# Performance work log

Hardware: AMD Instinct MI355X
Metric: run time of the kernel (lower is better)

## Reference

```python
import jax, jax.numpy as jnp
import numpy as np

B, T, J, V, D, H = 32, 400, 30, 50000, 150, 150
L = 2  # answer_token_len (boundary model: start, end)


def _gru_step(h, x, Wih, Whh, bih, bhh):
    # torch GRUCell semantics
    gi = x @ Wih.T + bih
    gh = h @ Whh.T + bhh
    ir, iz, inn = jnp.split(gi, 3, axis=-1)
    hr, hz, hn = jnp.split(gh, 3, axis=-1)
    r = jax.nn.sigmoid(ir + hr)
    z = jax.nn.sigmoid(iz + hz)
    n = jnp.tanh(inn + r * hn)
    return (1.0 - z) * n + z * h


def _gru_seq(x, Wih, Whh, bih, bhh):
    # x: [B, S, din] -> hidden sequence [B, S, h]
    h0 = jnp.zeros((x.shape[0], Whh.shape[1]), x.dtype)
    def step(h, xt):
        h = _gru_step(h, xt, Wih, Whh, bih, bhh)
        return h, h
    _, hs = jax.lax.scan(step, h0, jnp.swapaxes(x, 0, 1))
    return jnp.swapaxes(hs, 0, 1)


def _forward(context, query,
             E,
             ctx_Wih, ctx_Whh, ctx_bih, ctx_bhh,
             q_Wih, q_Whh, q_bih, q_bhh,
             Wq, Wp, Wr, w, gate_bias, attn_bias,
             m_Wih, m_Whh, m_bih, m_bhh,
             mr_Wih, mr_Whh, mr_bih, mr_bhh,
             ptr_W1, ptr_W2, ptr_v,
             d_Wih, d_Whh, d_bih, d_bhh):
    # encode context and query with GRUs
    Hp = _gru_seq(E[context], ctx_Wih, ctx_Whh, ctx_bih, ctx_bhh)  # [B,T,H]
    Hq = _gru_seq(E[query], q_Wih, q_Whh, q_bih, q_bhh)            # [B,J,H]

    whq = jnp.einsum('bjh,hk->bjk', Hq, Wq)  # precomputed query projection [B,J,H]

    def match_scan(xs, cWih, cWhh, cbih, cbhh):
        # xs: [B,T,H] context encodings (possibly time-reversed)
        def step(h, xt):
            # G_i = tanh(Wq Hq + (Wp p_i + Wr h_{i-1}) + bias)  -> [B,J,H]
            g = jnp.tanh(whq + (xt @ Wp + h @ Wr + gate_bias)[:, None, :])
            a = jax.nn.softmax(g @ w + attn_bias, axis=-1)       # [B,J]
            q = jnp.einsum('bj,bjh->bh', a, Hq)                  # attended query
            z = jnp.concatenate([xt, q], axis=-1)                # [B,2H]
            h = _gru_step(h, z, cWih, cWhh, cbih, cbhh)
            return h, h
        h0 = jnp.zeros((xs.shape[0], xs.shape[2]), xs.dtype)
        _, hs = jax.lax.scan(step, h0, jnp.swapaxes(xs, 0, 1))
        return jnp.swapaxes(hs, 0, 1)  # [B,T,H]

    Hf = match_scan(Hp, m_Wih, m_Whh, m_bih, m_bhh)              # forward direction
    Hb = match_scan(Hp[:, ::-1], mr_Wih, mr_Whh, mr_bih, mr_bhh) # reverse direction (scan order, as original)
    Hr = jnp.concatenate([Hf, Hb], axis=-1)                      # [B,T,2H]
    zero0 = jnp.zeros((Hr.shape[0], 1, Hr.shape[2]), Hr.dtype)   # initial zero state prepended
    Hr = jnp.concatenate([zero0, Hr], axis=1)                    # [B,T+1,2H]

    # boundary pointer network: L attention steps over H_r
    enc = Hr @ ptr_W1
    def ptr_step(h, _):
        s = jnp.tanh(enc + (h @ ptr_W2)[:, None, :]) @ ptr_v     # [B,T+1]
        a = jax.nn.softmax(s, axis=-1)
        c = jnp.einsum('bt,bth->bh', a, Hr)
        h = _gru_step(h, c, d_Wih, d_Whh, d_bih, d_bhh)
        return h, a
    h0 = jnp.zeros((Hr.shape[0], Hr.shape[2]), Hr.dtype)
    _, probs = jax.lax.scan(ptr_step, h0, None, length=L)
    return jnp.swapaxes(probs, 0, 1)  # [B, L, T+1]


def setup_inputs() -> dict:
    key = jax.random.key(0)
    keys = iter(jax.random.split(key, 40))
    p = lambda *s: jax.random.normal(next(keys), s, jnp.float32) * 0.05
    inp = {
        'context': jax.random.randint(next(keys), (B, T), 0, V, dtype=jnp.int32),
        'query': jax.random.randint(next(keys), (B, J), 0, V, dtype=jnp.int32),
        'E': p(V, D),
        'ctx_Wih': p(3 * H, D), 'ctx_Whh': p(3 * H, H), 'ctx_bih': p(3 * H), 'ctx_bhh': p(3 * H),
        'q_Wih': p(3 * H, D), 'q_Whh': p(3 * H, H), 'q_bih': p(3 * H), 'q_bhh': p(3 * H),
        'Wq': p(H, H), 'Wp': p(H, H), 'Wr': p(H, H), 'w': p(H),
        'gate_bias': p(H), 'attn_bias': p(),
        'm_Wih': p(3 * H, 2 * H), 'm_Whh': p(3 * H, H), 'm_bih': p(3 * H), 'm_bhh': p(3 * H),
        'mr_Wih': p(3 * H, 2 * H), 'mr_Whh': p(3 * H, H), 'mr_bih': p(3 * H), 'mr_bhh': p(3 * H),
        'ptr_W1': p(2 * H, 2 * H), 'ptr_W2': p(2 * H, 2 * H), 'ptr_v': p(2 * H),
        'd_Wih': p(6 * H, 2 * H), 'd_Whh': p(6 * H, 2 * H), 'd_bih': p(6 * H), 'd_bhh': p(6 * H),
    }
    return inp


def reference(context, query, E,
              ctx_Wih, ctx_Whh, ctx_bih, ctx_bhh,
              q_Wih, q_Whh, q_bih, q_bhh,
              Wq, Wp, Wr, w, gate_bias, attn_bias,
              m_Wih, m_Whh, m_bih, m_bhh,
              mr_Wih, mr_Whh, mr_bih, mr_bhh,
              ptr_W1, ptr_W2, ptr_v,
              d_Wih, d_Whh, d_bih, d_bhh):
    return _forward(context, query, E,
                    ctx_Wih, ctx_Whh, ctx_bih, ctx_bhh,
                    q_Wih, q_Whh, q_bih, q_bhh,
                    Wq, Wp, Wr, w, gate_bias, attn_bias,
                    m_Wih, m_Whh, m_bih, m_bhh,
                    mr_Wih, mr_Whh, mr_bih, mr_bhh,
                    ptr_W1, ptr_W2, ptr_v,
                    d_Wih, d_Whh, d_bih, d_bhh)
```

## Files before the change

### kernel.cpp

```cpp
#include <hip/hip_runtime.h>
#include <hip/hip_bf16.h>


namespace {

constexpr int NBATCH = 32;
constexpr int TLEN   = 400;
constexpr int JQ     = 30;
constexpr int T1     = 401;

__device__ __forceinline__ float sigm(float x){ return 1.f/(1.f+__expf(-x)); }
__device__ __forceinline__ float tanh_f(float x){
  float e = __expf(-2.f*fabsf(x));
  float t = (1.f-e)/(1.f+e);
  return x < 0.f ? -t : t;
}
__device__ __forceinline__ float bf2f(unsigned short u){
  union { unsigned int i; float f; } c; c.i = ((unsigned int)u)<<16; return c.f;
}

__device__ __forceinline__ void bar_lds(){
  asm volatile("s_waitcnt lgkmcnt(0)" ::: "memory");
  __builtin_amdgcn_s_barrier();
}

#define NW 29
struct WDesc { const void* src[NW]; int off[NW+1]; };

__global__ void sniff_kernel(const unsigned int* __restrict__ bits, int* __restrict__ flag){
  __shared__ int cnt;
  if (threadIdx.x==0) cnt = 0;
  __syncthreads();
  int hit = 0;
  #pragma unroll
  for (int i=0;i<4;i++){
    unsigned int w = bits[threadIdx.x*4+i];
    unsigned int b = (w>>8)&0x7Fu;
    if (b==0u || (b>=0x38u && b<=0x3Fu)) hit++;
  }
  atomicAdd(&cnt, hit);
  __syncthreads();
  if (threadIdx.x==0) *flag = (cnt > 768) ? 1 : 0;
}

__global__ void convert_weights_kernel(WDesc d, float* __restrict__ out, const int* __restrict__ flag){
  const int isbf = *flag;
  const int total = d.off[NW];
  for (int e = blockIdx.x*blockDim.x+threadIdx.x; e < total; e += gridDim.x*blockDim.x){
    int j = 0;
    while (e >= d.off[j+1]) j++;
    int i = e - d.off[j];
    out[e] = isbf ? bf2f(((const unsigned short*)d.src[j])[i])
                  : ((const float*)d.src[j])[i];
  }
}

__global__ void padrows_kernel(const float* __restrict__ src, float* __restrict__ dst,
                               int rows, int cols, int ldd){
  int i = blockIdx.x*blockDim.x+threadIdx.x;
  if (i >= rows*ldd) return;
  int r = i/ldd, c = i-r*ldd;
  dst[i] = (c<cols) ? src[(size_t)r*cols+c] : 0.f;
}

__global__ void transpose_kernel(const float* __restrict__ src, float* __restrict__ dst,
                                 int R, int C, int lds_, int offs){
  int idx = blockIdx.x*blockDim.x+threadIdx.x;
  if (idx >= R*C) return;
  int i = idx / R, k = idx - i*R;
  dst[(size_t)i*R + k] = src[(size_t)k*lds_ + offs + i];
}

__global__ void build_wcat_kernel(const float* __restrict__ Whh, const float* __restrict__ Wr,
                                  float* __restrict__ Wcat){
  int i = blockIdx.x*blockDim.x+threadIdx.x;
  if (i >= 600*152) return;
  int r = i/152, c = i-r*152;
  float v = 0.f;
  if (c < 150){
    if (r < 450) v = Whh[(size_t)r*150+c];
    else         v = Wr[(size_t)c*150 + (r-450)];
  }
  Wcat[i] = v;
}

__global__ void build_msplit_kernel(const float* __restrict__ Wcat,
                                    float* __restrict__ s2q, float* __restrict__ ext){
  int i = blockIdx.x*blockDim.x+threadIdx.x;
  if (i < 24576){
    int q = i/2048, rem = i-q*2048, r = rem/4, p = rem-r*4;
    s2q[i] = Wcat[(size_t)r*152 + 104 + 4*q + p];
  } else if (i < 24576+13376){
    int k = i-24576;
    int q = k/352, rem = k-q*352, ii = rem/4, p = rem-ii*4;
    ext[k] = Wcat[(size_t)(512+ii)*152 + 4*q + p];
  }
}

__global__ void build_gsplit_kernel(const float* __restrict__ Wpad, float* __restrict__ s2q){
  int i = blockIdx.x*blockDim.x+threadIdx.x;
  if (i >= 12*452*4) return;
  int q = i/1808, rem = i-q*1808, r = rem/4, p = rem-r*4;
  s2q[i] = (r<450) ? Wpad[(size_t)r*152 + 104 + 4*q + p] : 0.f;
}

__global__ __launch_bounds__(512) void rowproj16_kernel(
    const float* __restrict__ Xrows,
    const int* __restrict__ gather, const void* __restrict__ Etab, const int* __restrict__ bfflag,
    const float* __restrict__ W, const float* __restrict__ bias,
    float* __restrict__ out, int rows, int K, int inner, int ldw, int ldo)
{
  __shared__ __align__(16) float xs[16][304];
  const int r0 = blockIdx.x*16;
  int nr = rows - r0; if (nr > 16) nr = 16;
  if (nr <= 0) return;
  const int isbf = gather ? *bfflag : 0;
  for (int e = threadIdx.x; e < nr*inner; e += 512){
    int r = e/inner, i = e - r*inner;
    float v;
    if (gather){
      size_t base = (size_t)gather[r0+r]*inner + i;
      v = isbf ? bf2f(((const unsigned short*)Etab)[base]) : ((const float*)Etab)[base];
    } else {
      v = Xrows[(size_t)(r0+r)*inner + i];
    }
    xs[r][i] = v;
  }
  __syncthreads();
  for (int k = threadIdx.x; k < K; k += 512){
    float b0 = bias ? bias[k] : 0.f;
    float acc[16];
    #pragma unroll
    for (int r=0;r<16;r++) acc[r] = b0;
    int i = 0;
    for (; i+4 <= inner; i += 4){
      float w0 = W[(size_t)i*ldw + k];
      float w1 = W[(size_t)(i+1)*ldw + k];
      float w2 = W[(size_t)(i+2)*ldw + k];
      float w3 = W[(size_t)(i+3)*ldw + k];
      #pragma unroll
      for (int r=0;r<16;r++){
        float4 xv = *(const float4*)&xs[r][i];
        acc[r] = fmaf(xv.x, w0, acc[r]);
        acc[r] = fmaf(xv.y, w1, acc[r]);
        acc[r] = fmaf(xv.z, w2, acc[r]);
        acc[r] = fmaf(xv.w, w3, acc[r]);
      }
    }
    for (; i < inner; i++){
      float wv = W[(size_t)i*ldw + k];
      #pragma unroll
      for (int r=0;r<16;r++) acc[r] = fmaf(xs[r][i], wv, acc[r]);
    }
    for (int r=0;r<nr;r++) out[(size_t)(r0+r)*ldo + k] = acc[r];
  }
  for (int k = K + threadIdx.x; k < ldo; k += 512)
    for (int r=0;r<nr;r++) out[(size_t)(r0+r)*ldo + k] = 0.f;
}

#define R26(M) M(0) M(1) M(2) M(3) M(4) M(5) M(6) M(7) M(8) M(9) M(10) M(11) \
               M(12) M(13) M(14) M(15) M(16) M(17) M(18) M(19) M(20) M(21) \
               M(22) M(23) M(24) M(25)
#define R12(M) M(26) M(27) M(28) M(29) M(30) M(31) M(32) M(33) M(34) M(35) \
               M(36) M(37)
#define DECW(i) float4 w##i;
#define LDW(i)  w##i = wrow4[i];
#define LDW2(i) w##i = s2q4[(i-26)*s2stride + s2r];
#define FMAW(i) { float4 hq = h4[i]; \
  acc0 = fmaf(hq.x, w##i.x, acc0); acc1 = fmaf(hq.y, w##i.y, acc1); \
  acc2 = fmaf(hq.z, w##i.z, acc2); acc3 = fmaf(hq.w, w##i.w, acc3); }

__global__ __launch_bounds__(512, 2) void gru_scan_kernel(
    const float* __restrict__ gi0, const float* __restrict__ Wp0,
    const float* __restrict__ s2q0, const float* __restrict__ bh0,
    float* __restrict__ H0, int S0,
    const float* __restrict__ gi1, const float* __restrict__ Wp1,
    const float* __restrict__ s2q1, const float* __restrict__ bh1,
    float* __restrict__ H1, int S1)
{
  const int blk = blockIdx.x;
  const float* gi; const float* Wpad; const float* s2qG; const float* bh; float* Hs; int S;
  if (blk < 32){ gi = gi0 + (size_t)blk*S0*450;  Wpad = Wp0; s2qG = s2q0; bh = bh0;
                 Hs = H0 + (size_t)blk*S0*150;   S = S0; }
  else         { int bb = blk-32;
                 gi = gi1 + (size_t)bb*S1*450;   Wpad = Wp1; s2qG = s2q1; bh = bh1;
                 Hs = H1 + (size_t)bb*S1*150;    S = S1; }
  __shared__ __align__(16) float h[152];
  __shared__ float gh[452];
  const int tid = threadIdx.x;

  R26(DECW) R12(DECW)
  float br = 0.f;
  {
    const float4* wrow4 = (const float4*)(Wpad + (size_t)((tid<450)?tid:0)*152);
    R26(LDW)
    const float4* s2q4 = (const float4*)s2qG;
    const int s2stride = 452; const int s2r = (tid<452) ? tid : 0;
    R12(LDW2)
    if (tid<450) br = bh[tid];
  }
  if (tid < 152) h[tid] = 0.f;
  __syncthreads();
  const float4* h4 = (const float4*)h;

  for (int t=0;t<S;t++){
    float g0=0.f,g1=0.f,g2=0.f;
    if (tid < 150){
      const float* gg = gi + (size_t)t*450;
      g0 = gg[tid]; g1 = gg[150+tid]; g2 = gg[300+tid];
    }
    if (tid < 450){
      float acc0=br, acc1=0.f, acc2=0.f, acc3=0.f;
      R26(FMAW) R12(FMAW)
      gh[tid] = (acc0+acc2)+(acc1+acc3);
    }
    bar_lds();
    if (tid < 150){
      float r = sigm(g0 + gh[tid]);
      float z = sigm(g1 + gh[150+tid]);
      float n = tanh_f(g2 + r*gh[300+tid]);
      float hn = (1.f-z)*n + z*h[tid];
      h[tid] = hn;
      Hs[(size_t)t*150 + tid] = hn;
    }
    bar_lds();
  }
}

__global__ void zero_hr0_kernel(float* __restrict__ Hr){
  int idx = blockIdx.x*blockDim.x + threadIdx.x;
  if (idx < NBATCH*300){
    int b = idx/300, k = idx - 300*b;
    Hr[(size_t)b*T1*300 + k] = 0.f;
  }
}

__global__ __launch_bounds__(512, 2) void match_scan_kernel(
    const float* __restrict__ pWp,
    const float* __restrict__ whq,
    const float* __restrict__ giXf,
    const float* __restrict__ giXr,
    const float* __restrict__ Pf,
    const float* __restrict__ Pr,
    const float* __restrict__ WcatF, const float* __restrict__ WcatR,
    const float* __restrict__ s2qF,  const float* __restrict__ s2qR,
    const float* __restrict__ extF,  const float* __restrict__ extR,
    const float* __restrict__ m_bhh, const float* __restrict__ mr_bhh,
    const float* __restrict__ wvec,
    float* __restrict__ Hr)
{
  const int b   = blockIdx.x;
  const int dir = blockIdx.y;
  const float* giX  = dir ? giXr : giXf;
  const float* P    = dir ? Pr   : Pf;
  const float* Wcat = dir ? WcatR : WcatF;
  const float* s2qG = dir ? s2qR  : s2qF;
  const float* extG = dir ? extR  : extF;
  const float* bhh  = dir ? mr_bhh : m_bhh;

  __shared__ float4 extW[3344];
  __shared__ __align__(16) float Ps[JQ*452];
  __shared__ __align__(16) float whqS[JQ*152];
  __shared__ __align__(16) float wrP[760];
  __shared__ __align__(16) float h[152];
  __shared__ float ghsRaw[512];
  __shared__ __align__(16) float pwS[152];
  __shared__ __align__(16) float wlS[152];
  __shared__ float sc[32];

  const int tid  = threadIdx.x;
  const int lane = tid & 63;
  const int wv   = tid >> 6;
  const int er   = (tid < 440) ? (tid % 88) : 0;
  const int kg   = (tid < 440) ? (tid / 88) : 0;

  R26(DECW) R12(DECW)
  float br;
  {
    const float4* wrow4 = (const float4*)(Wcat + (size_t)tid*152);
    R26(LDW)
    const float4* s2q4 = (const float4*)s2qG;
    const int s2stride = 512; const int s2r = tid;
    R12(LDW2)
    br = (tid < 450) ? bhh[tid] : 0.f;
  }
  for (int e=tid; e<3344; e+=512) extW[e] = ((const float4*)extG)[e];
  {
    const float* Pb = P + (size_t)b*JQ*452;
    for (int e=tid; e<JQ*452; e+=512) Ps[e] = Pb[e];
    const float4* wq4 = (const float4*)(whq + (size_t)b*JQ*152);
    for (int e=tid; e<JQ*38; e+=512) ((float4*)whqS)[e] = wq4[e];
  }
  for (int e=tid; e<760; e+=512) wrP[e] = 0.f;
  if (tid < 152){
    h[tid] = 0.f;
    wlS[tid] = (tid<150) ? wvec[tid] : 0.f;
  }
  __syncthreads();
  const float4* h4 = (const float4*)h;
  const float4* wrP4 = (const float4*)wrP;

  for (int t=0;t<TLEN;t++){
    const int tt = dir ? (TLEN-1-t) : t;

    float gv0=0.f, gv1=0.f, gv2=0.f;
    if (tid < 150){
      const float* g = giX + ((size_t)b*TLEN + tt)*452;
      gv0 = g[tid]; gv1 = g[150+tid]; gv2 = g[300+tid];
    }
    float4 pwv;
    if (tid >= 440 && tid < 478)
      pwv = ((const float4*)(pWp + ((size_t)b*TLEN + tt)*152))[tid-440];

    {
      float acc0=br, acc1=0.f, acc2=0.f, acc3=0.f;
      R26(FMAW) R12(FMAW)
      float v = (acc0+acc2)+(acc1+acc3);
      ghsRaw[tid] = v;
      if (tid >= 450) wrP[tid-450] = v;
    }
    if (tid < 440){
      float e0=0.f, e1=0.f;
      #pragma unroll
      for (int j=0;j<8;j++){
        int q = kg*8+j;
        if (q < 38){
          float4 wq = extW[q*88+er]; float4 hq = h4[q];
          e0 = fmaf(hq.x,wq.x,e0); e1 = fmaf(hq.y,wq.y,e1);
          e0 = fmaf(hq.z,wq.z,e0); e1 = fmaf(hq.w,wq.w,e1);
        }
      }
      wrP[kg*152 + 62 + er] = e0+e1;
    }
    if (tid >= 440 && tid < 478) ((float4*)pwS)[tid-440] = pwv;
    bar_lds();

    {
      float4 b4; b4.x=b4.y=b4.z=b4.w=0.f;
      const bool bl = (lane < 38);
      if (bl){
        float4 pw4 = ((const float4*)pwS)[lane];
        float4 s0 = wrP4[lane],        s1 = wrP4[38+lane];
        float4 s2 = wrP4[76+lane],     s3 = wrP4[114+lane];
        float4 s4 = wrP4[152+lane];
        b4.x = pw4.x + s0.x+s1.x+s2.x+s3.x+s4.x;
        b4.y = pw4.y + s0.y+s1.y+s2.y+s3.y+s4.y;
        b4.z = pw4.z + s0.z+s1.z+s2.z+s3.z+s4.z;
        b4.w = pw4.w + s0.w+s1.w+s2.w+s3.w+s4.w;
      }
      #pragma unroll
      for (int jj=0;jj<4;jj++){
        int j = wv + 8*jj;
        float a = 0.f;
        if (j < JQ && bl){
          float4 q4 = ((const float4*)whqS)[j*38 + lane];
          float4 w4 = ((const float4*)wlS)[lane];
          a = w4.x*tanh_f(q4.x+b4.x);
          a = fmaf(w4.y, tanh_f(q4.y+b4.y), a);
          a = fmaf(w4.z, tanh_f(q4.z+b4.z), a);
          a = fmaf(w4.w, tanh_f(q4.w+b4.w), a);
        }
        #pragma unroll
        for (int off=32; off; off>>=1) a += __shfl_down(a, off);
        if (j < JQ && lane==0) sc[j] = a;
      }
    }
    bar_lds();

    if (tid < 192){
      float v = (lane < JQ) ? sc[lane] : -1e30f;
      float m = v;
      #pragma unroll
      for (int off=32; off; off>>=1) m = fmaxf(m, __shfl_down(m, off));
      m = __shfl(m, 0);
      float e = (lane < JQ) ? __expf(v-m) : 0.f;
      float su = e;
      #pragma unroll
      for (int off=32; off; off>>=1) su += __shfl_down(su, off);
      su = __shfl(su, 0);
      float aw = e/su;
      const int k = (tid < 150) ? tid : 0;
      float accr = gv0, accz = gv1, accn = gv2;
      #pragma unroll
      for (int j=0;j<JQ;j++){
        float aj = __shfl(aw, j);
        accr = fmaf(aj, Ps[j*452 + k],       accr);
        accz = fmaf(aj, Ps[j*452 + 150 + k], accz);
        accn = fmaf(aj, Ps[j*452 + 300 + k], accn);
      }
      if (tid < 150){
        float r = sigm(accr + ghsRaw[tid]);
        float z = sigm(accz + ghsRaw[150+tid]);
        float n = tanh_f(accn + r*ghsRaw[300+tid]);
        float hn = (1.f-z)*n + z*h[tid];
        h[tid] = hn;
        Hr[((size_t)b*T1 + (t+1))*300 + dir*150 + tid] = hn;
      }
    }
    bar_lds();
  }
}

__global__ __launch_bounds__(512,2) void ptr_scan_kernel(
    const float* __restrict__ enc, const float* __restrict__ Hr,
    const float* __restrict__ W2, const float* __restrict__ pv,
    const float* __restrict__ dWih, const float* __restrict__ dWhh,
    const float* __restrict__ dbih, const float* __restrict__ dbhh,
    void* __restrict__ outv, const int* __restrict__ flag)
{
  const int b = blockIdx.x;
  const int tid = threadIdx.x;
  const int isbf = *flag;
  __shared__ float h[300], hW2[300], sl[T1], al[T1], c[300];
  __shared__ float gis[900], ghs[900];
  __shared__ float vl[300];
  __shared__ float red[8];
  if (tid < 300){ h[tid] = 0.f; vl[tid] = pv[tid]; }
  __syncthreads();
  for (int l=0;l<2;l++){
    if (tid < 300){
      float a0=0.f,a1=0.f;
      for (int i=0;i<300;i+=2){
        a0 += h[i]  *W2[(size_t)i*300+tid];
        a1 += h[i+1]*W2[(size_t)(i+1)*300+tid];
      }
      hW2[tid] = a0+a1;
    }
    __syncthreads();
    {
      const int wv = tid>>6, lane = tid&63;
      for (int t=wv; t<T1; t+=8){
        const float* er = enc + ((size_t)b*T1 + t)*300;
        float acc = 0.f;
        for (int k=lane; k<300; k+=64) acc += vl[k]*tanh_f(er[k] + hW2[k]);
        #pragma unroll
        for (int off=32; off; off>>=1) acc += __shfl_down(acc, off);
        if (lane==0) sl[t] = acc;
      }
    }
    __syncthreads();
    {
      float v = (tid < T1) ? sl[tid] : -1e30f;
      float m = v;
      #pragma unroll
      for (int off=32; off; off>>=1) m = fmaxf(m, __shfl_down(m, off));
      if ((tid&63)==0) red[tid>>6] = m;
      __syncthreads();
      float bm = fmaxf(fmaxf(fmaxf(red[0],red[1]),fmaxf(red[2],red[3])),
                       fmaxf(fmaxf(red[4],red[5]),fmaxf(red[6],red[7])));
      float e = (tid < T1) ? __expf(v-bm) : 0.f;
      float su = e;
      #pragma unroll
      for (int off=32; off; off>>=1) su += __shfl_down(su, off);
      __syncthreads();
      if ((tid&63)==0) red[tid>>6] = su;
      __syncthreads();
      float bs = red[0]+red[1]+red[2]+red[3]+red[4]+red[5]+red[6]+red[7];
      if (tid < T1){
        float a = e/bs;
        al[tid] = a;
        size_t oi = ((size_t)b*2 + l)*T1 + tid;
        if (isbf) ((__hip_bfloat16*)outv)[oi] = __float2bfloat16(a);
        else      ((float*)outv)[oi] = a;
      }
    }
    __syncthreads();
    if (tid < 300){
      float acc = 0.f;
      for (int t=0;t<T1;t++) acc += al[t]*Hr[((size_t)b*T1 + t)*300 + tid];
      c[tid] = acc;
    }
    __syncthreads();
    for (int k=tid; k<900; k+=blockDim.x){
      const float* wi = dWih + (size_t)k*300;
      const float* wh = dWhh + (size_t)k*300;
      float a0 = dbih[k], a1 = dbhh[k];
      for (int i=0;i<300;i++){ a0 += c[i]*wi[i]; a1 += h[i]*wh[i]; }
      gis[k] = a0; ghs[k] = a1;
    }
    __syncthreads();
    if (tid < 300){
      float r = sigm(gis[tid] + ghs[tid]);
      float z = sigm(gis[300+tid] + ghs[300+tid]);
      float n = tanh_f(gis[600+tid] + r*ghs[600+tid]);
      h[tid] = (1.f-z)*n + z*h[tid];
    }
    __syncthreads();
  }
}

}

extern "C" void kernel_launch(void* const* d_in, const int* in_sizes, int n_in,
                              void* d_out, int out_size, void* d_ws, size_t ws_size,
                              hipStream_t stream)
{
  (void)in_sizes; (void)n_in; (void)out_size; (void)ws_size;
  float* ws = (float*)d_ws;
  int* flag = (int*)d_ws;

  static const int wsz[NW] = {
    67500,67500,450,450,
    67500,67500,450,450,
    22500,22500,22500,150,150,1,
    135000,67500,450,450,
    135000,67500,450,450,
    90000,90000,300,
    270000,270000,900,900
  };
  WDesc desc;
  int cum = 0;
  for (int j=0;j<NW;j++){ desc.src[j] = d_in[3+j]; desc.off[j] = cum; cum += wsz[j]; }
  desc.off[NW] = cum;

  float* WB = ws + 16;
  const float* P_ctx_Wih = WB + desc.off[0];
  const float* P_ctx_Whh = WB + desc.off[1];
  const float* P_ctx_bih = WB + desc.off[2];
  const float* P_ctx_bhh = WB + desc.off[3];
  const float* P_q_Wih   = WB + desc.off[4];
  const float* P_q_Whh   = WB + desc.off[5];
  const float* P_q_bih   = WB + desc.off[6];
  const float* P_q_bhh   = WB + desc.off[7];
  const float* P_Wq      = WB + desc.off[8];
  const float* P_Wp      = WB + desc.off[9];
  const float* P_Wr      = WB + desc.off[10];
  const float* P_w       = WB + desc.off[11];
  const float* P_gb      = WB + desc.off[12];
  const float* P_m_Wih   = WB + desc.off[14];
  const float* P_m_Whh   = WB + desc.off[15];
  const float* P_m_bih   = WB + desc.off[16];
  const float* P_m_bhh   = WB + desc.off[17];
  const float* P_mr_Wih  = WB + desc.off[18];
  const float* P_mr_Whh  = WB + desc.off[19];
  const float* P_mr_bih  = WB + desc.off[20];
  const float* P_mr_bhh  = WB + desc.off[21];
  const float* P_W1      = WB + desc.off[22];
  const float* P_W2      = WB + desc.off[23];
  const float* P_pv      = WB + desc.off[24];
  const float* P_dWih    = WB + desc.off[25];
  const float* P_dWhh    = WB + desc.off[26];
  const float* P_dbih    = WB + desc.off[27];
  const float* P_dbhh    = WB + desc.off[28];

  size_t p = 16 + 1468512;
  float* ctxWhhP = ws + p; p += 68400;
  float* qWhhP   = ws + p; p += 68400;
  float* s2qCtx  = ws + p; p += 21696;
  float* s2qQ    = ws + p; p += 21696;
  float* WcatF   = ws + p; p += 91200;
  float* WcatR   = ws + p; p += 91200;
  float* s2qF    = ws + p; p += 24576;
  float* s2qR    = ws + p; p += 24576;
  float* extFg   = ws + p; p += 13376;
  float* extRg   = ws + p; p += 13376;
  float* ctxWihT = ws + p; p += 67500;
  float* qWihT   = ws + p; p += 67500;
  float* mXfT    = ws + p; p += 67500;
  float* mXrT    = ws + p; p += 67500;
  float* mQfT    = ws + p; p += 67500;
  float* mQrT    = ws + p; p += 67500;

  float* ctx_gi = ws + p; p += 5760000;
  float* q_gi   = ws + p; p += 432000;
  float* HpB    = ws + p; p += 1920000;
  float* HqB    = ws + p; p += 144000;
  float* whqB   = ws + p; p += 145920;
  float* PfB    = ws + p; p += 433920;
  float* PrB    = ws + p; p += 433920;
  float* pWpB   = ws + p; p += 1945600;
  float* giXfB  = ws + p; p += 5785600;
  float* giXrB  = ws + p; p += 5785600;
  float* HrB    = ws + p; p += 3849600;
  float* encB   = ctx_gi;

  sniff_kernel<<<1,256,0,stream>>>((const unsigned int*)d_in[2], flag);
  convert_weights_kernel<<<512,256,0,stream>>>(desc, WB, flag);
  padrows_kernel<<<(450*152+255)/256,256,0,stream>>>(P_ctx_Whh, ctxWhhP, 450,150,152);
  padrows_kernel<<<(450*152+255)/256,256,0,stream>>>(P_q_Whh,   qWhhP,   450,150,152);
  build_gsplit_kernel<<<(12*452*4+255)/256,256,0,stream>>>(ctxWhhP, s2qCtx);
  build_gsplit_kernel<<<(12*452*4+255)/256,256,0,stream>>>(qWhhP,   s2qQ);
  build_wcat_kernel<<<(600*152+255)/256,256,0,stream>>>(P_m_Whh,  P_Wr, WcatF);
  build_wcat_kernel<<<(600*152+255)/256,256,0,stream>>>(P_mr_Whh, P_Wr, WcatR);
  build_msplit_kernel<<<(24576+13376+255)/256,256,0,stream>>>(WcatF, s2qF, extFg);
  build_msplit_kernel<<<(24576+13376+255)/256,256,0,stream>>>(WcatR, s2qR, extRg);
  transpose_kernel<<<(67500+255)/256,256,0,stream>>>(P_ctx_Wih, ctxWihT, 450,150,150,0);
  transpose_kernel<<<(67500+255)/256,256,0,stream>>>(P_q_Wih,   qWihT,   450,150,150,0);
  transpose_kernel<<<(67500+255)/256,256,0,stream>>>(P_m_Wih,   mXfT,    450,150,300,0);
  transpose_kernel<<<(67500+255)/256,256,0,stream>>>(P_mr_Wih,  mXrT,    450,150,300,0);
  transpose_kernel<<<(67500+255)/256,256,0,stream>>>(P_m_Wih,   mQfT,    450,150,300,150);
  transpose_kernel<<<(67500+255)/256,256,0,stream>>>(P_mr_Wih,  mQrT,    450,150,300,150);

  rowproj16_kernel<<<800,512,0,stream>>>(nullptr,(const int*)d_in[0], d_in[2], flag,
                                         ctxWihT, P_ctx_bih, ctx_gi, 12800,450,150,450,450);
  rowproj16_kernel<<<60,512,0,stream>>>(nullptr,(const int*)d_in[1], d_in[2], flag,
                                        qWihT, P_q_bih, q_gi, 960,450,150,450,450);

  gru_scan_kernel<<<64,512,0,stream>>>(ctx_gi, ctxWhhP, s2qCtx, P_ctx_bhh, HpB, 400,
                                       q_gi,   qWhhP,   s2qQ,   P_q_bhh,   HqB, 30);

  rowproj16_kernel<<<60,512,0,stream>>>(HqB,nullptr,nullptr,nullptr, P_Wq, nullptr,
                                        whqB, 960,150,150,150,152);
  rowproj16_kernel<<<60,512,0,stream>>>(HqB,nullptr,nullptr,nullptr, mQfT, nullptr,
                                        PfB, 960,450,150,450,452);
  rowproj16_kernel<<<60,512,0,stream>>>(HqB,nullptr,nullptr,nullptr, mQrT, nullptr,
                                        PrB, 960,450,150,450,452);
  rowproj16_kernel<<<800,512,0,stream>>>(HpB,nullptr,nullptr,nullptr, P_Wp, P_gb,
                                         pWpB, 12800,150,150,150,152);
  rowproj16_kernel<<<800,512,0,stream>>>(HpB,nullptr,nullptr,nullptr, mXfT, P_m_bih,
                                         giXfB, 12800,450,150,450,452);
  rowproj16_kernel<<<800,512,0,stream>>>(HpB,nullptr,nullptr,nullptr, mXrT, P_mr_bih,
                                         giXrB, 12800,450,150,450,452);

  zero_hr0_kernel<<<(NBATCH*300+511)/512,512,0,stream>>>(HrB);
  match_scan_kernel<<<dim3(NBATCH,2),512,0,stream>>>(pWpB, whqB, giXfB, giXrB,
                                                     PfB, PrB, WcatF, WcatR,
                                                     s2qF, s2qR, extFg, extRg,
                                                     P_m_bhh, P_mr_bhh, P_w, HrB);

  rowproj16_kernel<<<802,512,0,stream>>>(HrB,nullptr,nullptr,nullptr, P_W1, nullptr,
                                         encB, 12832,300,300,300,300);
  ptr_scan_kernel<<<32,512,0,stream>>>(encB, HrB, P_W2, P_pv,
                                       P_dWih, P_dWhh, P_dbih, P_dbhh, d_out, flag);
}
```

Measured before the change: 3.498 ms.

## Fuse weight prep kernels, batch row projections, and vectorize match-scan softmax

Replaces fourteen small weight-preparation launches with a single grid-stride prep kernel, and merges six row-projection launches into two kernels that load each input tile once and apply three weight matrices. Inside the match scan, the attention softmax is now computed per thread from float4 loads of the score buffer, with padding slots set to a large negative value, instead of wavefront shuffle reductions. The query projection tile is stored transposed (k-major, 32-padded j) so the weighted sum reads float4 vectors. The intent is to cut launch overhead, redundant input loads, and per-step shuffle latency on the serial scan, at the cost of a more complex prep indexing path with a branchy dispatch loop.

```diff
diff --git a/kernel.cpp b/kernel.cpp
--- a/kernel.cpp
+++ b/kernel.cpp
@@ -17,6 +17,14 @@
 }
 __device__ __forceinline__ float bf2f(unsigned short u){
   union { unsigned int i; float f; } c; c.i = ((unsigned int)u)<<16; return c.f;
+}
+__device__ __forceinline__ float q4max(float4 v){ return fmaxf(fmaxf(v.x,v.y),fmaxf(v.z,v.w)); }
+__device__ __forceinline__ float sum4(float4 v){ return (v.x+v.y)+(v.z+v.w); }
+__device__ __forceinline__ float4 exp4(float4 v, float m){
+  return make_float4(__expf(v.x-m),__expf(v.y-m),__expf(v.z-m),__expf(v.w-m));
+}
+__device__ __forceinline__ float4 scl4(float4 v, float s){
+  return make_float4(v.x*s,v.y*s,v.z*s,v.w*s);
 }
 
 __device__ __forceinline__ void bar_lds(){
@@ -55,53 +63,72 @@
   }
 }
 
-__global__ void padrows_kernel(const float* __restrict__ src, float* __restrict__ dst,
-                               int rows, int cols, int ldd){
-  int i = blockIdx.x*blockDim.x+threadIdx.x;
-  if (i >= rows*ldd) return;
-  int r = i/ldd, c = i-r*ldd;
-  dst[i] = (c<cols) ? src[(size_t)r*cols+c] : 0.f;
-}
-
-__global__ void transpose_kernel(const float* __restrict__ src, float* __restrict__ dst,
-                                 int R, int C, int lds_, int offs){
-  int idx = blockIdx.x*blockDim.x+threadIdx.x;
-  if (idx >= R*C) return;
-  int i = idx / R, k = idx - i*R;
-  dst[(size_t)i*R + k] = src[(size_t)k*lds_ + offs + i];
-}
-
-__global__ void build_wcat_kernel(const float* __restrict__ Whh, const float* __restrict__ Wr,
-                                  float* __restrict__ Wcat){
-  int i = blockIdx.x*blockDim.x+threadIdx.x;
-  if (i >= 600*152) return;
-  int r = i/152, c = i-r*152;
-  float v = 0.f;
-  if (c < 150){
-    if (r < 450) v = Whh[(size_t)r*150+c];
-    else         v = Wr[(size_t)c*150 + (r-450)];
-  }
-  Wcat[i] = v;
-}
-
-__global__ void build_msplit_kernel(const float* __restrict__ Wcat,
-                                    float* __restrict__ s2q, float* __restrict__ ext){
-  int i = blockIdx.x*blockDim.x+threadIdx.x;
-  if (i < 24576){
-    int q = i/2048, rem = i-q*2048, r = rem/4, p = rem-r*4;
-    s2q[i] = Wcat[(size_t)r*152 + 104 + 4*q + p];
-  } else if (i < 24576+13376){
-    int k = i-24576;
-    int q = k/352, rem = k-q*352, ii = rem/4, p = rem-ii*4;
-    ext[k] = Wcat[(size_t)(512+ii)*152 + 4*q + p];
-  }
-}
-
-__global__ void build_gsplit_kernel(const float* __restrict__ Wpad, float* __restrict__ s2q){
-  int i = blockIdx.x*blockDim.x+threadIdx.x;
-  if (i >= 12*452*4) return;
-  int q = i/1808, rem = i-q*1808, r = rem/4, p = rem-r*4;
-  s2q[i] = (r<450) ? Wpad[(size_t)r*152 + 104 + 4*q + p] : 0.f;
+struct PrepArgs {
+  const float *ctxWhh, *qWhh, *mWhh, *mrWhh, *Wr;
+  const float *ctxWih, *qWih, *mWih, *mrWih;
+  float *ctxWhhP, *qWhhP, *s2qCtx, *s2qQ, *WcatF, *WcatR, *s2qF, *s2qR;
+  float *extF, *extR, *ctxWihT, *qWihT, *mXfT, *mXrT, *mQfT, *mQrT;
+};
+
+__global__ void prep_all_kernel(PrepArgs a){
+  const int PN[16] = {68400,68400,21696,21696,91200,91200,24576,24576,
+                      13376,13376,67500,67500,67500,67500,67500,67500};
+  const int TOT = 843496;
+  for (int gid = blockIdx.x*blockDim.x+threadIdx.x; gid < TOT; gid += gridDim.x*blockDim.x){
+    int e = gid, t = 0;
+    while (e >= PN[t]){ e -= PN[t]; t++; }
+    switch (t){
+      case 0: case 1: {
+        const float* s = (t==0)? a.ctxWhh : a.qWhh;
+        float* d = (t==0)? a.ctxWhhP : a.qWhhP;
+        int r = e/152, c = e-r*152;
+        d[e] = (c<150) ? s[r*150+c] : 0.f;
+      } break;
+      case 2: case 3: {
+        const float* s = (t==2)? a.ctxWhh : a.qWhh;
+        float* d = (t==2)? a.s2qCtx : a.s2qQ;
+        int q = e/1808, rem = e-q*1808, r = rem/4, p = rem-r*4;
+        int c = 104 + 4*q + p;
+        d[e] = (r<450 && c<150) ? s[(size_t)r*150+c] : 0.f;
+      } break;
+      case 4: case 5: {
+        const float* s = (t==4)? a.mWhh : a.mrWhh;
+        float* d = (t==4)? a.WcatF : a.WcatR;
+        int r = e/152, c = e-r*152;
+        float v = 0.f;
+        if (c < 150) v = (r<450) ? s[(size_t)r*150+c] : a.Wr[(size_t)c*150 + (r-450)];
+        d[e] = v;
+      } break;
+      case 6: case 7: {
+        const float* s = (t==6)? a.mWhh : a.mrWhh;
+        float* d = (t==6)? a.s2qF : a.s2qR;
+        int q = e/2048, rem = e-q*2048, r = rem/4, p = rem-r*4;
+        int c = 104 + 4*q + p;
+        float v = 0.f;
+        if (c < 150) v = (r<450) ? s[(size_t)r*150+c] : a.Wr[(size_t)c*150 + (r-450)];
+        d[e] = v;
+      } break;
+      case 8: case 9: {
+        float* d = (t==8)? a.extF : a.extR;
+        int q = e/352, rem = e-q*352, ii = rem/4, p = rem-ii*4;
+        int c = 4*q + p;
+        d[e] = (c<150) ? a.Wr[(size_t)c*150 + 62 + ii] : 0.f;
+      } break;
+      default: {
+        int i2 = e/450, k = e-i2*450;
+        const float* s; float* d; int lds_, offs;
+        switch (t){
+          case 10: s=a.ctxWih; d=a.ctxWihT; lds_=150; offs=0;   break;
+          case 11: s=a.qWih;   d=a.qWihT;   lds_=150; offs=0;   break;
+          case 12: s=a.mWih;   d=a.mXfT;    lds_=300; offs=0;   break;
+          case 13: s=a.mrWih;  d=a.mXrT;    lds_=300; offs=0;   break;
+          case 14: s=a.mWih;   d=a.mQfT;    lds_=300; offs=150; break;
+          default: s=a.mrWih;  d=a.mQrT;    lds_=300; offs=150; break;
+        }
+        d[(size_t)i2*450 + k] = s[(size_t)k*lds_ + offs + i2];
+      } break;
+    }
+  }
 }
 
 __global__ __launch_bounds__(512) void rowproj16_kernel(
@@ -156,6 +183,73 @@
   }
   for (int k = K + threadIdx.x; k < ldo; k += 512)
     for (int r=0;r<nr;r++) out[(size_t)(r0+r)*ldo + k] = 0.f;
+}
+
+__device__ __forceinline__ void rowproj_one(
+    const float xs[16][152], int nr, int r0,
+    const float* __restrict__ W, const float* __restrict__ bias,
+    float* __restrict__ out, int K, int ldw, int ldo)
+{
+  for (int k = threadIdx.x; k < K; k += 512){
+    float b0 = bias ? bias[k] : 0.f;
+    float acc[16];
+    #pragma unroll
+    for (int r=0;r<16;r++) acc[r] = b0;
+    int i = 0;
+    for (; i+4 <= 148; i += 4){
+      float w0 = W[(size_t)i*ldw + k];
+      float w1 = W[(size_t)(i+1)*ldw + k];
+      float w2 = W[(size_t)(i+2)*ldw + k];
+      float w3 = W[(size_t)(i+3)*ldw + k];
+      #pragma unroll
+      for (int r=0;r<16;r++){
+        float4 xv = *(const float4*)&xs[r][i];
+        acc[r] = fmaf(xv.x, w0, acc[r]);
+        acc[r] = fmaf(xv.y, w1, acc[r]);
+        acc[r] = fmaf(xv.z, w2, acc[r]);
+        acc[r] = fmaf(xv.w, w3, acc[r]);
+      }
+    }
+    {
+      float w0 = W[(size_t)148*ldw + k];
+      float w1 = W[(size_t)149*ldw + k];
+      #pragma unroll
+      for (int r=0;r<16;r++){
+        acc[r] = fmaf(xs[r][148], w0, acc[r]);
+        acc[r] = fmaf(xs[r][149], w1, acc[r]);
+      }
+    }
+    for (int r=0;r<nr;r++) out[(size_t)(r0+r)*ldo + k] = acc[r];
+  }
+  for (int k = K + threadIdx.x; k < ldo; k += 512)
+    for (int r=0;r<nr;r++) out[(size_t)(r0+r)*ldo + k] = 0.f;
+}
+
+__global__ __launch_bounds__(512) void rowproj16_3_kernel(
+    const float* __restrict__ X, int rows,
+    const float* __restrict__ W0, const float* __restrict__ b0, float* __restrict__ o0,
+    int K0, int ldw0, int ldo0,
+    const float* __restrict__ W1, const float* __restrict__ b1, float* __restrict__ o1,
+    int K1, int ldw1, int ldo1,
+    const float* __restrict__ W2, const float* __restrict__ b2, float* __restrict__ o2,
+    int K2, int ldw2, int ldo2)
+{
+  __shared__ __align__(16) float xs[16][152];
+  const int r0 = blockIdx.x*16;
+  int nr = rows - r0; if (nr > 16) nr = 16;
+  if (nr <= 0) return;
+  for (int e = threadIdx.x; e < nr*150; e += 512){
+    int r = e/150, i = e - r*150;
+    xs[r][i] = X[(size_t)(r0+r)*150 + i];
+  }
+  if (threadIdx.x < 32){
+    int r = threadIdx.x/2, i = 150 + (threadIdx.x&1);
+    if (r < 16) xs[r][i] = 0.f;
+  }
+  __syncthreads();
+  rowproj_one(xs, nr, r0, W0, b0, o0, K0, ldw0, ldo0);
+  rowproj_one(xs, nr, r0, W1, b1, o1, K1, ldw1, ldo1);
+  rowproj_one(xs, nr, r0, W2, b2, o2, K2, ldw2, ldo2);
 }
 
 #define R26(M) M(0) M(1) M(2) M(3) M(4) M(5) M(6) M(7) M(8) M(9) M(10) M(11) \
@@ -259,15 +353,14 @@
   const float* bhh  = dir ? mr_bhh : m_bhh;
 
   __shared__ float4 extW[3344];
-  __shared__ __align__(16) float Ps[JQ*452];
+  __shared__ __align__(16) float PsT[15000];
   __shared__ __align__(16) float whqS[JQ*152];
   __shared__ __align__(16) float wrP[760];
   __shared__ __align__(16) float h[152];
   __shared__ float ghsRaw[512];
   __shared__ __align__(16) float pwS[152];
   __shared__ __align__(16) float wlS[152];
-  __shared__ float sc[32];
-
+  __shared__ __align__(16) float sc[32];
   const int tid  = threadIdx.x;
   const int lane = tid & 63;
   const int wv   = tid >> 6;
@@ -286,15 +379,26 @@
   }
   for (int e=tid; e<3344; e+=512) extW[e] = ((const float4*)extG)[e];
   {
-    const float* Pb = P + (size_t)b*JQ*452;
-    for (int e=tid; e<JQ*452; e+=512) Ps[e] = Pb[e];
     const float4* wq4 = (const float4*)(whq + (size_t)b*JQ*152);
     for (int e=tid; e<JQ*38; e+=512) ((float4*)whqS)[e] = wq4[e];
   }
-  for (int e=tid; e<760; e+=512) wrP[e] = 0.f;
+  for (int e=tid; e<15000; e+=512) PsT[e] = 0.f;
+  for (int e=tid; e<760;   e+=512) wrP[e] = 0.f;
   if (tid < 152){
     h[tid] = 0.f;
     wlS[tid] = (tid<150) ? wvec[tid] : 0.f;
+  }
+  if (tid >= 30 && tid < 32) sc[tid] = -1e30f;
+  __syncthreads();
+  {
+    const float* Pb = P + (size_t)b*JQ*452;
+    for (int e=tid; e<JQ*452; e+=512){
+      int j = e/452, kk = e - j*452;
+      if (kk < 450){
+        int g = kk/150, k = kk - g*150;
+        PsT[k*100 + g*32 + j] = Pb[e];
+      }
+    }
   }
   __syncthreads();
   const float4* h4 = (const float4*)h;
@@ -336,7 +440,7 @@
     bar_lds();
 
     {
-      float4 b4; b4.x=b4.y=b4.z=b4.w=0.f;
+      float4 b4 = make_float4(0.f,0.f,0.f,0.f);
       const bool bl = (lane < 38);
       if (bl){
         float4 pw4 = ((const float4*)pwS)[lane];
@@ -368,26 +472,30 @@
     bar_lds();
 
     if (tid < 192){
-      float v = (lane < JQ) ? sc[lane] : -1e30f;
-      float m = v;
-      #pragma unroll
-      for (int off=32; off; off>>=1) m = fmaxf(m, __shfl_down(m, off));
-      m = __shfl(m, 0);
-      float e = (lane < JQ) ? __expf(v-m) : 0.f;
-      float su = e;
-      #pragma unroll
-      for (int off=32; off; off>>=1) su += __shfl_down(su, off);
-      su = __shfl(su, 0);
-      float aw = e/su;
+      const float4* sc4 = (const float4*)sc;
+      float4 s0=sc4[0], s1=sc4[1], s2=sc4[2], s3=sc4[3];
+      float4 s4=sc4[4], s5=sc4[5], s6=sc4[6], s7=sc4[7];
+      float m = fmaxf(fmaxf(fmaxf(q4max(s0),q4max(s1)),fmaxf(q4max(s2),q4max(s3))),
+                      fmaxf(fmaxf(q4max(s4),q4max(s5)),fmaxf(q4max(s6),q4max(s7))));
+      float4 a0=exp4(s0,m), a1=exp4(s1,m), a2=exp4(s2,m), a3=exp4(s3,m);
+      float4 a4=exp4(s4,m), a5=exp4(s5,m), a6=exp4(s6,m), a7=exp4(s7,m);
+      float su = ((sum4(a0)+sum4(a1))+(sum4(a2)+sum4(a3)))
+               + ((sum4(a4)+sum4(a5))+(sum4(a6)+sum4(a7)));
+      float inv = 1.f/su;
+      a0=scl4(a0,inv); a1=scl4(a1,inv); a2=scl4(a2,inv); a3=scl4(a3,inv);
+      a4=scl4(a4,inv); a5=scl4(a5,inv); a6=scl4(a6,inv); a7=scl4(a7,inv);
       const int k = (tid < 150) ? tid : 0;
+      const float4* Pk = (const float4*)(PsT + k*100);
       float accr = gv0, accz = gv1, accn = gv2;
-      #pragma unroll
-      for (int j=0;j<JQ;j++){
-        float aj = __shfl(aw, j);
-        accr = fmaf(aj, Ps[j*452 + k],       accr);
-        accz = fmaf(aj, Ps[j*452 + 150 + k], accz);
-        accn = fmaf(aj, Ps[j*452 + 300 + k], accn);
-      }
+      #define ACC1(acc,P4,A4){ float4 p=P4; \
+        acc=fmaf(A4.x,p.x,acc); acc=fmaf(A4.y,p.y,acc); \
+        acc=fmaf(A4.z,p.z,acc); acc=fmaf(A4.w,p.w,acc); }
+      #define ACCG(acc,g){ ACC1(acc,Pk[g*8+0],a0) ACC1(acc,Pk[g*8+1],a1) \
+        ACC1(acc,Pk[g*8+2],a2) ACC1(acc,Pk[g*8+3],a3) ACC1(acc,Pk[g*8+4],a4) \
+        ACC1(acc,Pk[g*8+5],a5) ACC1(acc,Pk[g*8+6],a6) ACC1(acc,Pk[g*8+7],a7) }
+      ACCG(accr,0) ACCG(accz,1) ACCG(accn,2)
+      #undef ACC1
+      #undef ACCG
       if (tid < 150){
         float r = sigm(accr + ghsRaw[tid]);
         float z = sigm(accz + ghsRaw[150+tid]);
@@ -576,20 +684,16 @@
 
   sniff_kernel<<<1,256,0,stream>>>((const unsigned int*)d_in[2], flag);
   convert_weights_kernel<<<512,256,0,stream>>>(desc, WB, flag);
-  padrows_kernel<<<(450*152+255)/256,256,0,stream>>>(P_ctx_Whh, ctxWhhP, 450,150,152);
-  padrows_kernel<<<(450*152+255)/256,256,0,stream>>>(P_q_Whh,   qWhhP,   450,150,152);
-  build_gsplit_kernel<<<(12*452*4+255)/256,256,0,stream>>>(ctxWhhP, s2qCtx);
-  build_gsplit_kernel<<<(12*452*4+255)/256,256,0,stream>>>(qWhhP,   s2qQ);
-  build_wcat_kernel<<<(600*152+255)/256,256,0,stream>>>(P_m_Whh,  P_Wr, WcatF);
-  build_wcat_kernel<<<(600*152+255)/256,256,0,stream>>>(P_mr_Whh, P_Wr, WcatR);
-  build_msplit_kernel<<<(24576+13376+255)/256,256,0,stream>>>(WcatF, s2qF, extFg);
-  build_msplit_kernel<<<(24576+13376+255)/256,256,0,stream>>>(WcatR, s2qR, extRg);
-  transpose_kernel<<<(67500+255)/256,256,0,stream>>>(P_ctx_Wih, ctxWihT, 450,150,150,0);
-  transpose_kernel<<<(67500+255)/256,256,0,stream>>>(P_q_Wih,   qWihT,   450,150,150,0);
-  transpose_kernel<<<(67500+255)/256,256,0,stream>>>(P_m_Wih,   mXfT,    450,150,300,0);
-  transpose_kernel<<<(67500+255)/256,256,0,stream>>>(P_mr_Wih,  mXrT,    450,150,300,0);
-  transpose_kernel<<<(67500+255)/256,256,0,stream>>>(P_m_Wih,   mQfT,    450,150,300,150);
-  transpose_kernel<<<(67500+255)/256,256,0,stream>>>(P_mr_Wih,  mQrT,    450,150,300,150);
+  {
+    PrepArgs a;
+    a.ctxWhh = P_ctx_Whh; a.qWhh = P_q_Whh; a.mWhh = P_m_Whh; a.mrWhh = P_mr_Whh;
+    a.Wr = P_Wr; a.ctxWih = P_ctx_Wih; a.qWih = P_q_Wih; a.mWih = P_m_Wih; a.mrWih = P_mr_Wih;
+    a.ctxWhhP = ctxWhhP; a.qWhhP = qWhhP; a.s2qCtx = s2qCtx; a.s2qQ = s2qQ;
+    a.WcatF = WcatF; a.WcatR = WcatR; a.s2qF = s2qF; a.s2qR = s2qR;
+    a.extF = extFg; a.extR = extRg; a.ctxWihT = ctxWihT; a.qWihT = qWihT;
+    a.mXfT = mXfT; a.mXrT = mXrT; a.mQfT = mQfT; a.mQrT = mQrT;
+    prep_all_kernel<<<2048,256,0,stream>>>(a);
+  }
 
   rowproj16_kernel<<<800,512,0,stream>>>(nullptr,(const int*)d_in[0], d_in[2], flag,
                                          ctxWihT, P_ctx_bih, ctx_gi, 12800,450,150,450,450);
@@ -599,18 +703,14 @@
   gru_scan_kernel<<<64,512,0,stream>>>(ctx_gi, ctxWhhP, s2qCtx, P_ctx_bhh, HpB, 400,
                                        q_gi,   qWhhP,   s2qQ,   P_q_bhh,   HqB, 30);
 
-  rowproj16_kernel<<<60,512,0,stream>>>(HqB,nullptr,nullptr,nullptr, P_Wq, nullptr,
-                                        whqB, 960,150,150,150,152);
-  rowproj16_kernel<<<60,512,0,stream>>>(HqB,nullptr,nullptr,nullptr, mQfT, nullptr,
-                                        PfB, 960,450,150,450,452);
-  rowproj16_kernel<<<60,512,0,stream>>>(HqB,nullptr,nullptr,nullptr, mQrT, nullptr,
-                                        PrB, 960,450,150,450,452);
-  rowproj16_kernel<<<800,512,0,stream>>>(HpB,nullptr,nullptr,nullptr, P_Wp, P_gb,
-                                         pWpB, 12800,150,150,150,152);
-  rowproj16_kernel<<<800,512,0,stream>>>(HpB,nullptr,nullptr,nullptr, mXfT, P_m_bih,
-                                         giXfB, 12800,450,150,450,452);
-  rowproj16_kernel<<<800,512,0,stream>>>(HpB,nullptr,nullptr,nullptr, mXrT, P_mr_bih,
-                                         giXrB, 12800,450,150,450,452);
+  rowproj16_3_kernel<<<60,512,0,stream>>>(HqB, 960,
+      P_Wq, nullptr, whqB, 150, 150, 152,
+      mQfT, nullptr, PfB, 450, 450, 452,
+      mQrT, nullptr, PrB, 450, 450, 452);
+  rowproj16_3_kernel<<<800,512,0,stream>>>(HpB, 12800,
+      P_Wp, P_gb, pWpB, 150, 150, 152,
+      mXfT, P_m_bih, giXfB, 450, 450, 452,
+      mXrT, P_mr_bih, giXrB, 450, 450, 452);
 
   zero_hr0_kernel<<<(NBATCH*300+511)/512,512,0,stream>>>(HrB);
   match_scan_kernel<<<dim3(NBATCH,2),512,0,stream>>>(pWpB, whqB, giXfB, giXrB,
```

Result: faster. 3.197 ms (-8.6%).
